# Kernel tuning notes

Measured on AMD Instinct MI355X. Metric: run time of the kernel, lower is better.

## Reference

```python
import jax, jax.numpy as jnp
import numpy as np

B, T, FIN, D = 8, 512, 256, 128


def setup_inputs() -> dict:
    key = jax.random.key(0)
    ks = jax.random.split(key, 12)
    s = lambda fan_in: 1.0 / np.sqrt(fan_in)
    return {
        "x": jax.random.normal(ks[0], (B, T, FIN), jnp.float32),
        "S0": jnp.zeros((B, 1, D, D), jnp.float32),
        "Z0": jnp.zeros((B, 1, D), jnp.float32),
        "gamma": jnp.ones((FIN,), jnp.float32),
        "beta": jnp.zeros((FIN,), jnp.float32),
        "Wk": jax.random.normal(ks[1], (FIN, D), jnp.float32) * s(FIN),
        "Wq": jax.random.normal(ks[2], (FIN, D), jnp.float32) * s(FIN),
        "Wv": jax.random.normal(ks[3], (FIN, D), jnp.float32) * s(FIN),
        "W1": jax.random.normal(ks[4], (D, D), jnp.float32) * s(D),
        "b1": jnp.zeros((D,), jnp.float32),
        "W2": jax.random.normal(ks[5], (D, D), jnp.float32) * s(D),
        "b2": jnp.zeros((D,), jnp.float32),
        "Ws": jax.random.normal(ks[6], (FIN, D), jnp.float32) * s(FIN),
        "bs": jnp.zeros((D,), jnp.float32),
    }


def reference(x, S0, Z0, gamma, beta, Wk, Wq, Wv, W1, b1, W2, b2, Ws, bs):
    CLAMP = 1e20
    # LayerNorm over feature dim
    mu = jnp.mean(x, axis=-1, keepdims=True)
    var = jnp.var(x, axis=-1, keepdims=True)
    xn = (x - mu) / jnp.sqrt(var + 1e-5) * gamma + beta
    # phi(x) = elu(x) + 1
    K = jax.nn.elu(xn @ Wk) + 1.0  # [B,T,D]
    Q = jax.nn.elu(xn @ Wq) + 1.0  # [B,T,D]
    V = xn @ Wv                     # [B,T,D]
    # outer-product state recurrence via cumsum (faithful to original)
    outer = jnp.einsum('bti,btj->btij', K, V)            # [B,T,D,D]
    S = jnp.clip(jnp.cumsum(outer, axis=1), -CLAMP, CLAMP) + S0  # [B,T,D,D]
    Z = jnp.clip(jnp.cumsum(K, axis=1), -CLAMP, CLAMP) + Z0      # [B,T,D]
    numerator = jnp.einsum('bti,btil->btl', Q, S)        # [B,T,D]
    denominator = jnp.einsum('bti,bti->bt', Q, Z)[..., None] + 1e-5
    out = numerator / denominator
    # FFN: relu(relu(out W1 + b1) W2 + b2)
    out = jax.nn.relu(jax.nn.relu(out @ W1 + b1) @ W2 + b2)
    # residual shortcut from normed input
    out = out + xn @ Ws + bs
    S_out = S.reshape(B, T, D * D)
    return out, S_out, Z
```

## Files before the change

### kernel.cpp

```cpp
#include <hip/hip_runtime.h>


constexpr int BB = 8, TT = 512, FIN_ = 256, DD = 128;
constexpr int NROW = BB * TT;
constexpr int CLEN = 64, NCH = 8;
constexpr float CLAMPV = 1e20f;

typedef float f4v __attribute__((ext_vector_type(4)));

__global__ __launch_bounds__(256) void gemm_qkvs(
    const float* __restrict__ x,
    const float* __restrict__ gamma, const float* __restrict__ beta,
    const float* __restrict__ Wk, const float* __restrict__ Wq,
    const float* __restrict__ Wv, const float* __restrict__ Ws,
    const float* __restrict__ bs,
    float* __restrict__ Kb, float* __restrict__ Qb,
    float* __restrict__ Vb, float* __restrict__ Rb)
{
  int ct = blockIdx.x, rt = blockIdx.y;
  int mat = ct >> 1, cb = (ct & 1) * 64;
  const float* W = (mat == 0) ? Wk : (mat == 1) ? Wq : (mat == 2) ? Wv : Ws;
  float* Ob      = (mat == 0) ? Kb : (mat == 1) ? Qb : (mat == 2) ? Vb : Rb;
  __shared__ float As[16][64];
  __shared__ float Bs[16][64];
  __shared__ float mu_s[64], rs_s[64];
  int tid = threadIdx.x;
  {
    int row = tid >> 2, q = tid & 3;
    const float* xr = &x[(rt * 64 + row) * FIN_ + q * 64];
    float sum = 0.f, sq = 0.f;
#pragma unroll
    for (int u = 0; u < 16; u++) {
      float4 v = *(const float4*)&xr[u * 4];
      sum += v.x + v.y + v.z + v.w;
      sq  += v.x * v.x + v.y * v.y + v.z * v.z + v.w * v.w;
    }
    sum += __shfl_xor(sum, 1); sq += __shfl_xor(sq, 1);
    sum += __shfl_xor(sum, 2); sq += __shfl_xor(sq, 2);
    if (q == 0) {
      float mu = sum * (1.0f / FIN_);
      float var = sq * (1.0f / FIN_) - mu * mu;
      mu_s[row] = mu;
      rs_s[row] = rsqrtf(var + 1e-5f);
    }
  }
  __syncthreads();
  int tn = tid & 15, tm = tid >> 4;
  int lm = tid >> 2, lq = tid & 3;
  int lk = tid >> 4, ln4 = (tid & 15) * 4;
  float acc[4][4] = {};
  float mu = mu_s[lm], rs = rs_s[lm];
  for (int k0 = 0; k0 < FIN_; k0 += 16) {
    float4 av = *(const float4*)&x[(rt * 64 + lm) * FIN_ + k0 + lq * 4];
    float4 g  = *(const float4*)&gamma[k0 + lq * 4];
    float4 be = *(const float4*)&beta[k0 + lq * 4];
    As[lq * 4 + 0][lm] = (av.x - mu) * rs * g.x + be.x;
    As[lq * 4 + 1][lm] = (av.y - mu) * rs * g.y + be.y;
    As[lq * 4 + 2][lm] = (av.z - mu) * rs * g.z + be.z;
    As[lq * 4 + 3][lm] = (av.w - mu) * rs * g.w + be.w;
    *(float4*)&Bs[lk][ln4] = *(const float4*)&W[(k0 + lk) * DD + cb + ln4];
    __syncthreads();
#pragma unroll
    for (int k = 0; k < 16; k++) {
      float4 a = *(const float4*)&As[k][tm * 4];
      float4 b = *(const float4*)&Bs[k][tn * 4];
      float ar[4] = {a.x, a.y, a.z, a.w};
      float br[4] = {b.x, b.y, b.z, b.w};
#pragma unroll
      for (int i = 0; i < 4; i++)
#pragma unroll
        for (int j = 0; j < 4; j++) acc[i][j] += ar[i] * br[j];
    }
    __syncthreads();
  }
#pragma unroll
  for (int i = 0; i < 4; i++) {
    int row = rt * 64 + tm * 4 + i;
    int col = cb + tn * 4;
    float vals[4];
#pragma unroll
    for (int j = 0; j < 4; j++) {
      float v = acc[i][j];
      if (mat <= 1) v = (v > 0.f) ? v + 1.f : expf(v);
      else if (mat == 3) v += bs[col + j];
      vals[j] = v;
    }
    float4 o = make_float4(vals[0], vals[1], vals[2], vals[3]);
    *(float4*)&Ob[row * DD + col] = o;
  }
}

__global__ __launch_bounds__(256) void prefix_kernel(
    const float* __restrict__ Kb, const float* __restrict__ Vb,
    const float* __restrict__ S0, const float* __restrict__ Z0,
    float* __restrict__ prefS, float* __restrict__ prefz)
{
  int jt = blockIdx.x, it = blockIdx.y, b = blockIdx.z;
  int i0 = it * 16, j0 = jt * 32;
  __shared__ float Ks[CLEN][16];
  __shared__ float Vs[CLEN][32];
  int tid = threadIdx.x;
  int il = tid >> 4, jl = tid & 15;
  float2 s0v = *(const float2*)&S0[b * DD * DD + (i0 + il) * DD + j0 + jl * 2];
  float acc0 = 0.f, acc1 = 0.f;
  float zacc = 0.f;
  float z0v = (jt == 0 && tid < 16) ? Z0[b * DD + i0 + tid] : 0.f;
  for (int c = 0; c < NCH; c++) {
    const float* Kc = Kb + (b * TT + c * CLEN) * DD;
    const float* Vc = Vb + (b * TT + c * CLEN) * DD;
    {
      int t = tid >> 2, i4 = (tid & 3) * 4;
      *(float4*)&Ks[t][i4] = *(const float4*)&Kc[t * DD + i0 + i4];
    }
#pragma unroll
    for (int u = 0; u < 2; u++) {
      int idx = u * 256 + tid;
      int t = idx >> 3, j4 = (idx & 7) * 4;
      *(float4*)&Vs[t][j4] = *(const float4*)&Vc[t * DD + j0 + j4];
    }
    __syncthreads();
    float2 op = make_float2(acc0 + s0v.x, acc1 + s0v.y);
    *(float2*)&prefS[(size_t)(b * NCH + c) * DD * DD + (i0 + il) * DD + j0 + jl * 2] = op;
    if (jt == 0 && tid < 16)
      prefz[(b * NCH + c) * DD + i0 + tid] = zacc + z0v;
#pragma unroll 8
    for (int t = 0; t < CLEN; t++) {
      float k = Ks[t][il];
      float2 v2 = *(const float2*)&Vs[t][jl * 2];
      acc0 += k * v2.x;
      acc1 += k * v2.y;
    }
    if (jt == 0 && tid < 16) {
      float z = 0.f;
#pragma unroll 8
      for (int t = 0; t < CLEN; t++) z += Ks[t][tid];
      zacc += z;
    }
    __syncthreads();
  }
}

__global__ __launch_bounds__(256) void attn_kernel(
    const float* __restrict__ Kb, const float* __restrict__ Qb,
    const float* __restrict__ Vb, const float* __restrict__ prefS,
    const float* __restrict__ prefz,
    float* __restrict__ Zout, float* __restrict__ attn_o)
{
  int sub = blockIdx.x, c = blockIdx.y, b = blockIdx.z, tid = threadIdx.x;
  int t0 = sub * 8;
  int tlim = t0 + 8;
  __shared__ float KsT[DD][CLEN + 2];
  __shared__ float Qs[8][132];
  __shared__ float sc[8][CLEN + 2];
  __shared__ float zeff[DD];
  __shared__ float den[8];
  const float* Kc = Kb + (b * TT + c * CLEN) * DD;
  const float* Qc = Qb + (b * TT + c * CLEN) * DD;
  const float* Vc = Vb + (b * TT + c * CLEN) * DD;
  for (int idx = tid; idx < tlim * 32; idx += 256) {
    int t = idx >> 5, c4 = (idx & 31) * 4;
    float4 v = *(const float4*)&Kc[t * DD + c4];
    KsT[c4 + 0][t] = v.x; KsT[c4 + 1][t] = v.y;
    KsT[c4 + 2][t] = v.z; KsT[c4 + 3][t] = v.w;
  }
  {
    int r = tid >> 5, c4 = (tid & 31) * 4;
    float4 q = *(const float4*)&Qc[(t0 + r) * DD + c4];
    *(float4*)&Qs[r][c4] = q;
  }
  if (tid < DD) zeff[tid] = prefz[(b * NCH + c) * DD + tid];
  __syncthreads();
  {
    int tm = tid >> 5, tn = tid & 31;
    int tau0 = tn * 2;
    if (tau0 < tlim) {
      float s0 = 0.f, s1 = 0.f;
#pragma unroll 8
      for (int k = 0; k < DD; k++) {
        float q = Qs[tm][k];
        float2 kk = *(const float2*)&KsT[k][tau0];
        s0 += q * kk.x;
        s1 += q * kk.y;
      }
      int t = t0 + tm;
      sc[tm][tau0]     = (tau0     <= t) ? s0 : 0.f;
      sc[tm][tau0 + 1] = (tau0 + 1 <= t) ? s1 : 0.f;
    }
  }
  __syncthreads();
  if (tid < 8) {
    int t = t0 + tid;
    float d = 0.f;
    for (int tau = 0; tau <= t; tau++) d += sc[tid][tau];
    float dz = 0.f;
#pragma unroll 8
    for (int k = 0; k < DD; k++) dz += Qs[tid][k] * zeff[k];
    den[tid] = d + dz + 1e-5f;
  }
  __syncthreads();
  int tl = tid & 31, r = tid >> 5;
  int l0 = tl * 4;
  float n0[4] = {};
#pragma unroll 4
  for (int tau = 0; tau < tlim; tau++) {
    float4 v4 = *(const float4*)&Vc[tau * DD + l0];
    float s = sc[r][tau];
    n0[0] += s * v4.x; n0[1] += s * v4.y; n0[2] += s * v4.z; n0[3] += s * v4.w;
  }
  const float* P = prefS + (size_t)(b * NCH + c) * DD * DD;
#pragma unroll 4
  for (int i = 0; i < DD; i++) {
    float4 p4 = *(const float4*)&P[i * DD + l0];
    float q = Qs[r][i];
    n0[0] += q * p4.x; n0[1] += q * p4.y; n0[2] += q * p4.z; n0[3] += q * p4.w;
  }
  float* og = attn_o + (size_t)(b * TT + c * CLEN + t0) * DD;
  {
    float dd = den[r];
    float4 o = make_float4(n0[0] / dd, n0[1] / dd, n0[2] / dd, n0[3] / dd);
    *(float4*)&og[r * DD + l0] = o;
  }
  if (sub == 7 && tid < DD) {
    int i = tid;
    float a = zeff[i];
    for (int t = 0; t < CLEN; t++) {
      a += KsT[i][t];
      a = fminf(fmaxf(a, -CLAMPV), CLAMPV);
      __builtin_nontemporal_store(a, &Zout[(size_t)(b * TT + c * CLEN + t) * DD + i]);
    }
  }
}

__global__ __launch_bounds__(256) void ffn_kernel(
    const float* __restrict__ att, const float* __restrict__ res,
    const float* __restrict__ W1, const float* __restrict__ b1,
    const float* __restrict__ W2, const float* __restrict__ b2,
    float* __restrict__ outp)
{
  int rt = blockIdx.x, tid = threadIdx.x;
  __shared__ float As[16][132];
  __shared__ float H1[16][132];
  const float* ab = att + rt * 16 * DD;
  {
    int idx = tid;
#pragma unroll
    for (int u = 0; u < 2; u++, idx += 256) {
      int r = idx >> 5, c4 = (idx & 31) * 4;
      *(float4*)&As[r][c4] = *(const float4*)&ab[r * DD + c4];
    }
  }
  __syncthreads();
  int cn = tid & 31, rm = tid >> 5;
  int col = cn * 4, r0 = rm * 2;
  float acc[2][4] = {};
#pragma unroll 8
  for (int k = 0; k < DD; k++) {
    float4 w = *(const float4*)&W1[k * DD + col];
    float a0 = As[r0][k], a1 = As[r0 + 1][k];
    acc[0][0] += a0 * w.x; acc[0][1] += a0 * w.y; acc[0][2] += a0 * w.z; acc[0][3] += a0 * w.w;
    acc[1][0] += a1 * w.x; acc[1][1] += a1 * w.y; acc[1][2] += a1 * w.z; acc[1][3] += a1 * w.w;
  }
  float4 bv = *(const float4*)&b1[col];
#pragma unroll
  for (int i = 0; i < 2; i++) {
    float4 h;
    h.x = fmaxf(acc[i][0] + bv.x, 0.f);
    h.y = fmaxf(acc[i][1] + bv.y, 0.f);
    h.z = fmaxf(acc[i][2] + bv.z, 0.f);
    h.w = fmaxf(acc[i][3] + bv.w, 0.f);
    *(float4*)&H1[r0 + i][col] = h;
  }
  __syncthreads();
  float acc2[2][4] = {};
#pragma unroll 8
  for (int k = 0; k < DD; k++) {
    float4 w = *(const float4*)&W2[k * DD + col];
    float a0 = H1[r0][k], a1 = H1[r0 + 1][k];
    acc2[0][0] += a0 * w.x; acc2[0][1] += a0 * w.y; acc2[0][2] += a0 * w.z; acc2[0][3] += a0 * w.w;
    acc2[1][0] += a1 * w.x; acc2[1][1] += a1 * w.y; acc2[1][2] += a1 * w.z; acc2[1][3] += a1 * w.w;
  }
  float4 b2v = *(const float4*)&b2[col];
#pragma unroll
  for (int i = 0; i < 2; i++) {
    int row = rt * 16 + r0 + i;
    float4 rv = *(const float4*)&res[row * DD + col];
    float4 o;
    o.x = fmaxf(acc2[i][0] + b2v.x, 0.f) + rv.x;
    o.y = fmaxf(acc2[i][1] + b2v.y, 0.f) + rv.y;
    o.z = fmaxf(acc2[i][2] + b2v.z, 0.f) + rv.z;
    o.w = fmaxf(acc2[i][3] + b2v.w, 0.f) + rv.w;
    *(float4*)&outp[row * DD + col] = o;
  }
}

__global__ __launch_bounds__(512) void s_write_kernel(
    const float* __restrict__ Kb, const float* __restrict__ Vb,
    const float* __restrict__ prefS, float* __restrict__ Sout)
{
  int it = blockIdx.x, c = blockIdx.y, b = blockIdx.z;
  int i0 = it * 16;
  __shared__ float Vs[CLEN][DD];
  __shared__ float Ksm[CLEN][16];
  int tid = threadIdx.x;
  const float* Kc = Kb + (b * TT + c * CLEN) * DD;
  const float* Vc = Vb + (b * TT + c * CLEN) * DD;
#pragma unroll
  for (int u = 0; u < 4; u++) {
    int idx = u * 512 + tid;
    int t = idx >> 5, c4 = (idx & 31) * 4;
    *(float4*)&Vs[t][c4] = *(const float4*)&Vc[t * DD + c4];
  }
#pragma unroll
  for (int u = 0; u < 2; u++) {
    int idx = u * 512 + tid;
    int t = idx >> 4, r = idx & 15;
    Ksm[t][r] = Kc[t * DD + i0 + r];
  }
  __syncthreads();
  int irow = tid >> 5, jq = tid & 31;
  int j = jq * 4;
  float4 pref = *(const float4*)&prefS[(size_t)(b * NCH + c) * DD * DD + (i0 + irow) * DD + j];
  float4 acc = make_float4(0.f, 0.f, 0.f, 0.f);
  float* So = Sout + (size_t)(b * TT + c * CLEN) * (DD * DD) + (i0 + irow) * DD + j;
#pragma unroll 4
  for (int t = 0; t < CLEN; t++) {
    float4 v4 = *(const float4*)&Vs[t][j];
    float kk = Ksm[t][irow];
    acc.x += kk * v4.x; acc.y += kk * v4.y;
    acc.z += kk * v4.z; acc.w += kk * v4.w;
    f4v o4;
    o4.x = fminf(fmaxf(pref.x + acc.x, -CLAMPV), CLAMPV);
    o4.y = fminf(fmaxf(pref.y + acc.y, -CLAMPV), CLAMPV);
    o4.z = fminf(fmaxf(pref.z + acc.z, -CLAMPV), CLAMPV);
    o4.w = fminf(fmaxf(pref.w + acc.w, -CLAMPV), CLAMPV);
    __builtin_nontemporal_store(o4, (f4v*)&So[(size_t)t * (DD * DD)]);
  }
}

extern "C" void kernel_launch(void* const* d_in, const int* in_sizes, int n_in,
                              void* d_out, int out_size, void* d_ws, size_t ws_size,
                              hipStream_t stream)
{
  const float* x     = (const float*)d_in[0];
  const float* S0    = (const float*)d_in[1];
  const float* Z0    = (const float*)d_in[2];
  const float* gamma = (const float*)d_in[3];
  const float* beta  = (const float*)d_in[4];
  const float* Wk    = (const float*)d_in[5];
  const float* Wq    = (const float*)d_in[6];
  const float* Wv    = (const float*)d_in[7];
  const float* W1    = (const float*)d_in[8];
  const float* b1    = (const float*)d_in[9];
  const float* W2    = (const float*)d_in[10];
  const float* b2    = (const float*)d_in[11];
  const float* Ws    = (const float*)d_in[12];
  const float* bs    = (const float*)d_in[13];

  float* out_main = (float*)d_out;
  float* Sout = out_main + NROW * DD;
  float* Zout = Sout + (size_t)NROW * DD * DD;

  float* ws_f   = (float*)d_ws;
  float* Kb     = ws_f;
  float* Qb     = Kb + 524288;
  float* Vb     = Qb + 524288;
  float* Rb     = Vb + 524288;
  float* prefS  = Rb + 524288;
  float* prefz  = prefS + 1048576;
  float* attn_o = prefz + 8192;

  gemm_qkvs<<<dim3(8, 64), 256, 0, stream>>>(x, gamma, beta, Wk, Wq, Wv, Ws, bs,
                                             Kb, Qb, Vb, Rb);
  prefix_kernel<<<dim3(4, 8, BB), 256, 0, stream>>>(Kb, Vb, S0, Z0, prefS, prefz);
  attn_kernel<<<dim3(8, NCH, BB), 256, 0, stream>>>(Kb, Qb, Vb, prefS, prefz, Zout, attn_o);
  ffn_kernel<<<NROW / 16, 256, 0, stream>>>(attn_o, Rb, W1, b1, W2, b2, out_main);
  s_write_kernel<<<dim3(8, NCH, BB), 512, 0, stream>>>(Kb, Vb, prefS, Sout);
}
```

Baseline: 402.2 us.

## Fuse attention, FFN and S-write into one heterogeneous mega kernel

Merges the attention, FFN and S-output writing kernels into one launch. Blocks with blockIdx.x >= 8 write the S state (8 rows each, 256 threads), and the remaining blocks compute attention and then the FFN directly from shared memory, which removes the attn_o round trip through global memory and two launches. The S-write work now runs at the same time as the attention/FFN blocks. The trade-off is a larger shared-memory union per block, which can lower occupancy, and FFN weights are now reread by 512 blocks of 8 rows each instead of 256 blocks of 16 rows.

```diff
diff --git a/kernel.cpp b/kernel.cpp
--- a/kernel.cpp
+++ b/kernel.cpp
@@ -140,35 +140,89 @@
   }
 }
 
-__global__ __launch_bounds__(256) void attn_kernel(
+union MegaSmem {
+  struct {
+    float KsT[DD][CLEN + 2];
+    float Qs[8][132];
+    float sc[8][CLEN + 2];
+    float zeff[DD];
+    float den[8];
+    float As[8][132];
+    float H1[8][132];
+  } a;
+  struct {
+    float Vs[CLEN][DD];
+    float Ksm[CLEN][8];
+  } s;
+};
+
+__global__ __launch_bounds__(256) void mega_kernel(
     const float* __restrict__ Kb, const float* __restrict__ Qb,
     const float* __restrict__ Vb, const float* __restrict__ prefS,
-    const float* __restrict__ prefz,
-    float* __restrict__ Zout, float* __restrict__ attn_o)
+    const float* __restrict__ prefz, const float* __restrict__ Rb,
+    const float* __restrict__ W1, const float* __restrict__ b1,
+    const float* __restrict__ W2, const float* __restrict__ b2,
+    float* __restrict__ Zout, float* __restrict__ out_main,
+    float* __restrict__ Sout)
 {
-  int sub = blockIdx.x, c = blockIdx.y, b = blockIdx.z, tid = threadIdx.x;
+  __shared__ MegaSmem sm;
+  int c = blockIdx.y, b = blockIdx.z, tid = threadIdx.x;
+  const float* Kc = Kb + (b * TT + c * CLEN) * DD;
+  const float* Vc = Vb + (b * TT + c * CLEN) * DD;
+
+  if (blockIdx.x >= 8) {
+    int it = blockIdx.x - 8;
+    int i0 = it * 8;
+#pragma unroll
+    for (int u = 0; u < 8; u++) {
+      int idx = u * 256 + tid;
+      int t = idx >> 5, c4 = (idx & 31) * 4;
+      *(float4*)&sm.s.Vs[t][c4] = *(const float4*)&Vc[t * DD + c4];
+    }
+#pragma unroll
+    for (int u = 0; u < 2; u++) {
+      int idx = u * 256 + tid;
+      int t = idx >> 3, r = idx & 7;
+      sm.s.Ksm[t][r] = Kc[t * DD + i0 + r];
+    }
+    __syncthreads();
+    int irow = tid >> 5, jq = tid & 31;
+    int j = jq * 4;
+    float4 pref = *(const float4*)&prefS[(size_t)(b * NCH + c) * DD * DD + (i0 + irow) * DD + j];
+    float4 acc = make_float4(0.f, 0.f, 0.f, 0.f);
+    float* So = Sout + (size_t)(b * TT + c * CLEN) * (DD * DD) + (i0 + irow) * DD + j;
+#pragma unroll 4
+    for (int t = 0; t < CLEN; t++) {
+      float4 v4 = *(const float4*)&sm.s.Vs[t][j];
+      float kk = sm.s.Ksm[t][irow];
+      acc.x += kk * v4.x; acc.y += kk * v4.y;
+      acc.z += kk * v4.z; acc.w += kk * v4.w;
+      f4v o4;
+      o4.x = fminf(fmaxf(pref.x + acc.x, -CLAMPV), CLAMPV);
+      o4.y = fminf(fmaxf(pref.y + acc.y, -CLAMPV), CLAMPV);
+      o4.z = fminf(fmaxf(pref.z + acc.z, -CLAMPV), CLAMPV);
+      o4.w = fminf(fmaxf(pref.w + acc.w, -CLAMPV), CLAMPV);
+      __builtin_nontemporal_store(o4, (f4v*)&So[(size_t)t * (DD * DD)]);
+    }
+    return;
+  }
+
+  int sub = blockIdx.x;
   int t0 = sub * 8;
   int tlim = t0 + 8;
-  __shared__ float KsT[DD][CLEN + 2];
-  __shared__ float Qs[8][132];
-  __shared__ float sc[8][CLEN + 2];
-  __shared__ float zeff[DD];
-  __shared__ float den[8];
-  const float* Kc = Kb + (b * TT + c * CLEN) * DD;
   const float* Qc = Qb + (b * TT + c * CLEN) * DD;
-  const float* Vc = Vb + (b * TT + c * CLEN) * DD;
   for (int idx = tid; idx < tlim * 32; idx += 256) {
     int t = idx >> 5, c4 = (idx & 31) * 4;
     float4 v = *(const float4*)&Kc[t * DD + c4];
-    KsT[c4 + 0][t] = v.x; KsT[c4 + 1][t] = v.y;
-    KsT[c4 + 2][t] = v.z; KsT[c4 + 3][t] = v.w;
+    sm.a.KsT[c4 + 0][t] = v.x; sm.a.KsT[c4 + 1][t] = v.y;
+    sm.a.KsT[c4 + 2][t] = v.z; sm.a.KsT[c4 + 3][t] = v.w;
   }
   {
     int r = tid >> 5, c4 = (tid & 31) * 4;
     float4 q = *(const float4*)&Qc[(t0 + r) * DD + c4];
-    *(float4*)&Qs[r][c4] = q;
-  }
-  if (tid < DD) zeff[tid] = prefz[(b * NCH + c) * DD + tid];
+    *(float4*)&sm.a.Qs[r][c4] = q;
+  }
+  if (tid < DD) sm.a.zeff[tid] = prefz[(b * NCH + c) * DD + tid];
   __syncthreads();
   {
     int tm = tid >> 5, tn = tid & 31;
@@ -177,163 +231,92 @@
       float s0 = 0.f, s1 = 0.f;
 #pragma unroll 8
       for (int k = 0; k < DD; k++) {
-        float q = Qs[tm][k];
-        float2 kk = *(const float2*)&KsT[k][tau0];
+        float q = sm.a.Qs[tm][k];
+        float2 kk = *(const float2*)&sm.a.KsT[k][tau0];
         s0 += q * kk.x;
         s1 += q * kk.y;
       }
       int t = t0 + tm;
-      sc[tm][tau0]     = (tau0     <= t) ? s0 : 0.f;
-      sc[tm][tau0 + 1] = (tau0 + 1 <= t) ? s1 : 0.f;
+      sm.a.sc[tm][tau0]     = (tau0     <= t) ? s0 : 0.f;
+      sm.a.sc[tm][tau0 + 1] = (tau0 + 1 <= t) ? s1 : 0.f;
     }
   }
   __syncthreads();
   if (tid < 8) {
     int t = t0 + tid;
     float d = 0.f;
-    for (int tau = 0; tau <= t; tau++) d += sc[tid][tau];
+    for (int tau = 0; tau <= t; tau++) d += sm.a.sc[tid][tau];
     float dz = 0.f;
 #pragma unroll 8
-    for (int k = 0; k < DD; k++) dz += Qs[tid][k] * zeff[k];
-    den[tid] = d + dz + 1e-5f;
+    for (int k = 0; k < DD; k++) dz += sm.a.Qs[tid][k] * sm.a.zeff[k];
+    sm.a.den[tid] = d + dz + 1e-5f;
   }
   __syncthreads();
   int tl = tid & 31, r = tid >> 5;
   int l0 = tl * 4;
-  float n0[4] = {};
+  {
+    float n0[4] = {};
 #pragma unroll 4
-  for (int tau = 0; tau < tlim; tau++) {
-    float4 v4 = *(const float4*)&Vc[tau * DD + l0];
-    float s = sc[r][tau];
-    n0[0] += s * v4.x; n0[1] += s * v4.y; n0[2] += s * v4.z; n0[3] += s * v4.w;
-  }
-  const float* P = prefS + (size_t)(b * NCH + c) * DD * DD;
+    for (int tau = 0; tau < tlim; tau++) {
+      float4 v4 = *(const float4*)&Vc[tau * DD + l0];
+      float s = sm.a.sc[r][tau];
+      n0[0] += s * v4.x; n0[1] += s * v4.y; n0[2] += s * v4.z; n0[3] += s * v4.w;
+    }
+    const float* P = prefS + (size_t)(b * NCH + c) * DD * DD;
 #pragma unroll 4
-  for (int i = 0; i < DD; i++) {
-    float4 p4 = *(const float4*)&P[i * DD + l0];
-    float q = Qs[r][i];
-    n0[0] += q * p4.x; n0[1] += q * p4.y; n0[2] += q * p4.z; n0[3] += q * p4.w;
-  }
-  float* og = attn_o + (size_t)(b * TT + c * CLEN + t0) * DD;
-  {
-    float dd = den[r];
+    for (int i = 0; i < DD; i++) {
+      float4 p4 = *(const float4*)&P[i * DD + l0];
+      float q = sm.a.Qs[r][i];
+      n0[0] += q * p4.x; n0[1] += q * p4.y; n0[2] += q * p4.z; n0[3] += q * p4.w;
+    }
+    float dd = sm.a.den[r];
     float4 o = make_float4(n0[0] / dd, n0[1] / dd, n0[2] / dd, n0[3] / dd);
-    *(float4*)&og[r * DD + l0] = o;
+    *(float4*)&sm.a.As[r][l0] = o;
   }
   if (sub == 7 && tid < DD) {
     int i = tid;
-    float a = zeff[i];
+    float a = sm.a.zeff[i];
     for (int t = 0; t < CLEN; t++) {
-      a += KsT[i][t];
+      a += sm.a.KsT[i][t];
       a = fminf(fmaxf(a, -CLAMPV), CLAMPV);
       __builtin_nontemporal_store(a, &Zout[(size_t)(b * TT + c * CLEN + t) * DD + i]);
     }
   }
-}
-
-__global__ __launch_bounds__(256) void ffn_kernel(
-    const float* __restrict__ att, const float* __restrict__ res,
-    const float* __restrict__ W1, const float* __restrict__ b1,
-    const float* __restrict__ W2, const float* __restrict__ b2,
-    float* __restrict__ outp)
-{
-  int rt = blockIdx.x, tid = threadIdx.x;
-  __shared__ float As[16][132];
-  __shared__ float H1[16][132];
-  const float* ab = att + rt * 16 * DD;
-  {
-    int idx = tid;
-#pragma unroll
-    for (int u = 0; u < 2; u++, idx += 256) {
-      int r = idx >> 5, c4 = (idx & 31) * 4;
-      *(float4*)&As[r][c4] = *(const float4*)&ab[r * DD + c4];
-    }
-  }
-  __syncthreads();
-  int cn = tid & 31, rm = tid >> 5;
-  int col = cn * 4, r0 = rm * 2;
-  float acc[2][4] = {};
-#pragma unroll 8
-  for (int k = 0; k < DD; k++) {
-    float4 w = *(const float4*)&W1[k * DD + col];
-    float a0 = As[r0][k], a1 = As[r0 + 1][k];
-    acc[0][0] += a0 * w.x; acc[0][1] += a0 * w.y; acc[0][2] += a0 * w.z; acc[0][3] += a0 * w.w;
-    acc[1][0] += a1 * w.x; acc[1][1] += a1 * w.y; acc[1][2] += a1 * w.z; acc[1][3] += a1 * w.w;
-  }
-  float4 bv = *(const float4*)&b1[col];
-#pragma unroll
-  for (int i = 0; i < 2; i++) {
+  __syncthreads();
+  {
+    float a1[4] = {};
+#pragma unroll 8
+    for (int k = 0; k < DD; k++) {
+      float4 w = *(const float4*)&W1[k * DD + l0];
+      float a = sm.a.As[r][k];
+      a1[0] += a * w.x; a1[1] += a * w.y; a1[2] += a * w.z; a1[3] += a * w.w;
+    }
+    float4 bv = *(const float4*)&b1[l0];
     float4 h;
-    h.x = fmaxf(acc[i][0] + bv.x, 0.f);
-    h.y = fmaxf(acc[i][1] + bv.y, 0.f);
-    h.z = fmaxf(acc[i][2] + bv.z, 0.f);
-    h.w = fmaxf(acc[i][3] + bv.w, 0.f);
-    *(float4*)&H1[r0 + i][col] = h;
-  }
-  __syncthreads();
-  float acc2[2][4] = {};
-#pragma unroll 8
-  for (int k = 0; k < DD; k++) {
-    float4 w = *(const float4*)&W2[k * DD + col];
-    float a0 = H1[r0][k], a1 = H1[r0 + 1][k];
-    acc2[0][0] += a0 * w.x; acc2[0][1] += a0 * w.y; acc2[0][2] += a0 * w.z; acc2[0][3] += a0 * w.w;
-    acc2[1][0] += a1 * w.x; acc2[1][1] += a1 * w.y; acc2[1][2] += a1 * w.z; acc2[1][3] += a1 * w.w;
-  }
-  float4 b2v = *(const float4*)&b2[col];
-#pragma unroll
-  for (int i = 0; i < 2; i++) {
-    int row = rt * 16 + r0 + i;
-    float4 rv = *(const float4*)&res[row * DD + col];
+    h.x = fmaxf(a1[0] + bv.x, 0.f);
+    h.y = fmaxf(a1[1] + bv.y, 0.f);
+    h.z = fmaxf(a1[2] + bv.z, 0.f);
+    h.w = fmaxf(a1[3] + bv.w, 0.f);
+    *(float4*)&sm.a.H1[r][l0] = h;
+  }
+  __syncthreads();
+  {
+    float a2[4] = {};
+#pragma unroll 8
+    for (int k = 0; k < DD; k++) {
+      float4 w = *(const float4*)&W2[k * DD + l0];
+      float a = sm.a.H1[r][k];
+      a2[0] += a * w.x; a2[1] += a * w.y; a2[2] += a * w.z; a2[3] += a * w.w;
+    }
+    int grow = b * TT + c * CLEN + t0 + r;
+    float4 b2v = *(const float4*)&b2[l0];
+    float4 rv = *(const float4*)&Rb[grow * DD + l0];
     float4 o;
-    o.x = fmaxf(acc2[i][0] + b2v.x, 0.f) + rv.x;
-    o.y = fmaxf(acc2[i][1] + b2v.y, 0.f) + rv.y;
-    o.z = fmaxf(acc2[i][2] + b2v.z, 0.f) + rv.z;
-    o.w = fmaxf(acc2[i][3] + b2v.w, 0.f) + rv.w;
-    *(float4*)&outp[row * DD + col] = o;
-  }
-}
-
-__global__ __launch_bounds__(512) void s_write_kernel(
-    const float* __restrict__ Kb, const float* __restrict__ Vb,
-    const float* __restrict__ prefS, float* __restrict__ Sout)
-{
-  int it = blockIdx.x, c = blockIdx.y, b = blockIdx.z;
-  int i0 = it * 16;
-  __shared__ float Vs[CLEN][DD];
-  __shared__ float Ksm[CLEN][16];
-  int tid = threadIdx.x;
-  const float* Kc = Kb + (b * TT + c * CLEN) * DD;
-  const float* Vc = Vb + (b * TT + c * CLEN) * DD;
-#pragma unroll
-  for (int u = 0; u < 4; u++) {
-    int idx = u * 512 + tid;
-    int t = idx >> 5, c4 = (idx & 31) * 4;
-    *(float4*)&Vs[t][c4] = *(const float4*)&Vc[t * DD + c4];
-  }
-#pragma unroll
-  for (int u = 0; u < 2; u++) {
-    int idx = u * 512 + tid;
-    int t = idx >> 4, r = idx & 15;
-    Ksm[t][r] = Kc[t * DD + i0 + r];
-  }
-  __syncthreads();
-  int irow = tid >> 5, jq = tid & 31;
-  int j = jq * 4;
-  float4 pref = *(const float4*)&prefS[(size_t)(b * NCH + c) * DD * DD + (i0 + irow) * DD + j];
-  float4 acc = make_float4(0.f, 0.f, 0.f, 0.f);
-  float* So = Sout + (size_t)(b * TT + c * CLEN) * (DD * DD) + (i0 + irow) * DD + j;
-#pragma unroll 4
-  for (int t = 0; t < CLEN; t++) {
-    float4 v4 = *(const float4*)&Vs[t][j];
-    float kk = Ksm[t][irow];
-    acc.x += kk * v4.x; acc.y += kk * v4.y;
-    acc.z += kk * v4.z; acc.w += kk * v4.w;
-    f4v o4;
-    o4.x = fminf(fmaxf(pref.x + acc.x, -CLAMPV), CLAMPV);
-    o4.y = fminf(fmaxf(pref.y + acc.y, -CLAMPV), CLAMPV);
-    o4.z = fminf(fmaxf(pref.z + acc.z, -CLAMPV), CLAMPV);
-    o4.w = fminf(fmaxf(pref.w + acc.w, -CLAMPV), CLAMPV);
-    __builtin_nontemporal_store(o4, (f4v*)&So[(size_t)t * (DD * DD)]);
+    o.x = fmaxf(a2[0] + b2v.x, 0.f) + rv.x;
+    o.y = fmaxf(a2[1] + b2v.y, 0.f) + rv.y;
+    o.z = fmaxf(a2[2] + b2v.z, 0.f) + rv.z;
+    o.w = fmaxf(a2[3] + b2v.w, 0.f) + rv.w;
+    *(float4*)&out_main[grow * DD + l0] = o;
   }
 }
 
@@ -367,12 +350,11 @@
   float* Rb     = Vb + 524288;
   float* prefS  = Rb + 524288;
   float* prefz  = prefS + 1048576;
-  float* attn_o = prefz + 8192;
 
   gemm_qkvs<<<dim3(8, 64), 256, 0, stream>>>(x, gamma, beta, Wk, Wq, Wv, Ws, bs,
                                              Kb, Qb, Vb, Rb);
   prefix_kernel<<<dim3(4, 8, BB), 256, 0, stream>>>(Kb, Vb, S0, Z0, prefS, prefz);
-  attn_kernel<<<dim3(8, NCH, BB), 256, 0, stream>>>(Kb, Qb, Vb, prefS, prefz, Zout, attn_o);
-  ffn_kernel<<<NROW / 16, 256, 0, stream>>>(attn_o, Rb, W1, b1, W2, b2, out_main);
-  s_write_kernel<<<dim3(8, NCH, BB), 512, 0, stream>>>(Kb, Vb, prefS, Sout);
+  mega_kernel<<<dim3(24, NCH, BB), 256, 0, stream>>>(Kb, Qb, Vb, prefS, prefz, Rb,
+                                                     W1, b1, W2, b2,
+                                                     Zout, out_main, Sout);
 }
```

New measurement: 381.9 us. 1.05x faster.
